# Kernel tuning notes

Hardware: AMD Instinct MI355X
Metric: run time of the kernel (lower is better)

## Reference

```python
import jax, jax.numpy as jnp
import numpy as np

D_IN = 1024
D_OUT = 1024
NUM_HEADS = 16
HEAD_DIM = D_OUT // NUM_HEADS


def setup_inputs() -> dict:
    key = jax.random.key(0)
    ks = jax.random.split(key, 9)
    s = 0.02
    return {
        "x": jax.random.normal(ks[0], (2, 2048, D_IN), dtype=jnp.float32),
        "Wq": jax.random.normal(ks[1], (D_IN, D_OUT), dtype=jnp.float32) * s,
        "bq": jnp.zeros((D_OUT,), dtype=jnp.float32),
        "Wk": jax.random.normal(ks[2], (D_IN, D_OUT), dtype=jnp.float32) * s,
        "bk": jnp.zeros((D_OUT,), dtype=jnp.float32),
        "Wv": jax.random.normal(ks[3], (D_IN, D_OUT), dtype=jnp.float32) * s,
        "bv": jnp.zeros((D_OUT,), dtype=jnp.float32),
        "Wo": jax.random.normal(ks[4], (D_OUT, D_OUT), dtype=jnp.float32) * s,
        "bo": jnp.zeros((D_OUT,), dtype=jnp.float32),
    }


def reference(x, Wq, bq, Wk, bk, Wv, bv, Wo, bo):
    B, S, _ = x.shape
    H, Dh = NUM_HEADS, HEAD_DIM
    q = (x @ Wq + bq).reshape(B, S, H, Dh).transpose(0, 2, 1, 3)  # bhsd
    k = (x @ Wk + bk).reshape(B, S, H, Dh).transpose(0, 2, 1, 3)
    v = (x @ Wv + bv).reshape(B, S, H, Dh).transpose(0, 2, 1, 3)
    scores = jnp.einsum("bhqd,bhkd->bhqk", q, k) * (Dh ** -0.5)
    causal = jnp.tril(jnp.ones((S, S), dtype=bool))
    scores = jnp.where(causal, scores, jnp.float32(-jnp.inf))
    w = jax.nn.softmax(scores, axis=-1)
    ctx = jnp.einsum("bhqk,bhkd->bhqd", w, v)
    ctx = ctx.transpose(0, 2, 1, 3).reshape(B, S, H * Dh)
    return ctx @ Wo + bo
```

## Files before the change

kernel.cpp:

```cpp
#include <hip/hip_runtime.h>
#include <cmath>

#define D_IN 1024
#define D_OUT 1024
#define NUM_HEADS 16
#define HEAD_DIM 64
#define BATCH 2
#define SEQ 2048
#define GK 1024
#define KT 32
#define NT_K (GK / 64)

typedef __attribute__((ext_vector_type(8))) short short8;
typedef __attribute__((ext_vector_type(4))) short short4v;
typedef __attribute__((ext_vector_type(4))) float float4v;
typedef __attribute__((ext_vector_type(16))) float f32x16;
typedef __attribute__((ext_vector_type(2))) int int2v;

__device__ __forceinline__ unsigned short f2bf(float f) {
  unsigned int u = __builtin_bit_cast(unsigned int, f);
  unsigned int r = (u + 0x7FFFu + ((u >> 16) & 1u)) >> 16;
  return (unsigned short)r;
}
__device__ __forceinline__ float bf2f(unsigned short h) {
  return __builtin_bit_cast(float, (unsigned int)h << 16);
}

__device__ __forceinline__ unsigned int cvtpk(float lo, float hi) {
  unsigned int r;
  asm("v_cvt_pk_bf16_f32 %0, %1, %2" : "=v"(r) : "v"(lo), "v"(hi));
  return r;
}

__device__ __forceinline__ void async_copy16(void* lds, const void* g) {
  __builtin_amdgcn_global_load_lds(
      (const __attribute__((address_space(1))) unsigned int*)g,
      (__attribute__((address_space(3))) unsigned int*)lds, 16, 0, 0);
}

__global__ __launch_bounds__(256) void prep(
    const float* __restrict__ x, const float* __restrict__ Wq,
    const float* __restrict__ Wk, const float* __restrict__ Wv,
    const float* __restrict__ Wo, unsigned short* __restrict__ xb,
    unsigned short* __restrict__ wqkv_t, unsigned short* __restrict__ wo_t) {
  const int z = blockIdx.z;
  if (z == 4) {
    const int bid = blockIdx.y * 32 + blockIdx.x;
    const size_t i0 = ((size_t)bid * 256 + threadIdx.x) * 16;
#pragma unroll
    for (int half = 0; half < 2; ++half) {
      const size_t o = i0 + half * 8;
      float4 a = *(const float4*)(x + o);
      float4 b = *(const float4*)(x + o + 4);
      union { unsigned int d[4]; short8 v; } t;
      t.d[0] = cvtpk(a.x, a.y); t.d[1] = cvtpk(a.z, a.w);
      t.d[2] = cvtpk(b.x, b.y); t.d[3] = cvtpk(b.z, b.w);
      *(short8*)(xb + o) = t.v;
    }
    return;
  }
  const float* W = (z == 0) ? Wq : (z == 1) ? Wk : (z == 2) ? Wv : Wo;
  unsigned short* out = (z < 3) ? (wqkv_t + (size_t)z * 1024 * 1024) : wo_t;

  __shared__ float T[32][33];
  const int r = threadIdx.x >> 3;
  const int c4 = (threadIdx.x & 7) << 2;
  const int k0 = blockIdx.x * 32, n0 = blockIdx.y * 32;

  float4 v = *(const float4*)(W + (size_t)(k0 + r) * 1024 + n0 + c4);
  T[r][c4 + 0] = v.x; T[r][c4 + 1] = v.y; T[r][c4 + 2] = v.z; T[r][c4 + 3] = v.w;
  __syncthreads();

  union { unsigned short u[4]; short4v v4; } o;
#pragma unroll
  for (int i = 0; i < 4; ++i) o.u[i] = f2bf(T[c4 + i][r]);
  *(short4v*)(out + (size_t)(n0 + r) * 1024 + k0 + c4) = o.v4;
}

__device__ __forceinline__ void stage_tile(
    const unsigned short* __restrict__ A, const unsigned short* __restrict__ Bt,
    unsigned short* S, int buf, int bm, int bn, int k0, int wave, int lane) {
  unsigned short* As = S + buf * 16384;
  unsigned short* Bs = As + 8192;
#pragma unroll
  for (int t = 0; t < 4; ++t) {
    const int c = (wave * 4 + t) * 64 + lane;
    const int srow = c >> 3;
    const int sgc = ((c & 7) ^ (srow & 7)) * 8;
    async_copy16(As + (size_t)c * 8, A + (size_t)(bm + srow) * GK + k0 + sgc);
  }
#pragma unroll
  for (int t = 0; t < 4; ++t) {
    const int c = (wave * 4 + t) * 64 + lane;
    const int srow = c >> 3;
    const int sgc = ((c & 7) ^ (srow & 7)) * 8;
    async_copy16(Bs + (size_t)c * 8, Bt + (size_t)(bn + srow) * GK + k0 + sgc);
  }
}

__device__ __forceinline__ void gemm_core(
    const unsigned short* __restrict__ A, const unsigned short* __restrict__ Bt,
    unsigned short* S, int bm, int bn, float4v acc[4][4]) {
  const int tid = threadIdx.x;
  const int wave = tid >> 6, lane = tid & 63;
  const int quad = lane >> 4, l16 = lane & 15;
  const int wr = wave >> 1, wc = wave & 1;
  const int sw = l16 & 7;

  stage_tile(A, Bt, S, 0, bm, bn, 0, wave, lane);

  for (int t = 0; t < NT_K; ++t) {
    if (t + 1 < NT_K) {
      stage_tile(A, Bt, S, (t + 1) & 1, bm, bn, (t + 1) * 64, wave, lane);
      asm volatile("s_waitcnt vmcnt(8)" ::: "memory");
    } else {
      asm volatile("s_waitcnt vmcnt(0)" ::: "memory");
    }
    __builtin_amdgcn_sched_barrier(0);
    __builtin_amdgcn_s_barrier();
    __builtin_amdgcn_sched_barrier(0);

    const unsigned short* Asc = S + (t & 1) * 16384;
    const unsigned short* Bsc = Asc + 8192;
#pragma unroll
    for (int h = 0; h < 2; ++h) {
      short8 af[4], bfr[4];
#pragma unroll
      for (int i = 0; i < 4; ++i) {
        const int row = wr * 64 + i * 16 + l16;
        af[i] = *(const short8*)&Asc[((size_t)row * 8 + ((h * 4 + quad) ^ sw)) * 8];
      }
#pragma unroll
      for (int j = 0; j < 4; ++j) {
        const int row = wc * 64 + j * 16 + l16;
        bfr[j] = *(const short8*)&Bsc[((size_t)row * 8 + ((h * 4 + quad) ^ sw)) * 8];
      }
#pragma unroll
      for (int i = 0; i < 4; ++i)
#pragma unroll
        for (int j = 0; j < 4; ++j)
          acc[i][j] = __builtin_amdgcn_mfma_f32_16x16x32_bf16(af[i], bfr[j], acc[i][j], 0, 0, 0);
    }

    __builtin_amdgcn_sched_barrier(0);
    __builtin_amdgcn_s_barrier();
    __builtin_amdgcn_sched_barrier(0);
  }
}

__global__ __launch_bounds__(256) void gemm_qkv(
    const unsigned short* __restrict__ A, const unsigned short* __restrict__ Bt,
    const float* __restrict__ bq, const float* __restrict__ bk,
    const float* __restrict__ bv,
    unsigned short* __restrict__ qbuf, unsigned short* __restrict__ kblk,
    unsigned short* __restrict__ vblk) {
  __shared__ unsigned short SMEM[2 * 128 * 64 * 2];
  const int tid = threadIdx.x;
  const int wave = tid >> 6, lane = tid & 63;
  const int quad = lane >> 4, l16 = lane & 15;
  const int wr = wave >> 1, wc = wave & 1;

  const int lid = blockIdx.y * 32 + blockIdx.x;
  const int nid = (lid & 7) * 96 + (lid >> 3);
  const int bm = (nid & 31) * 128, bn = (nid >> 5) * 128;

  float4v acc[4][4] = {};
  gemm_core(A, Bt, SMEM, bm, bn, acc);

  __syncthreads();

  const int seg = bn >> 10;
  const int nb0 = bn & 1023;
  const float* bias = (seg == 0) ? bq : (seg == 1) ? bk : bv;
  const float scale = (seg == 0) ? 0.18033688011112043f : 1.0f;

#pragma unroll
  for (int j = 0; j < 4; ++j) {
    const int nl = wc * 64 + j * 16 + l16;
    const float bsv = bias[nb0 + nl];
#pragma unroll
    for (int i = 0; i < 4; ++i) {
#pragma unroll
      for (int r = 0; r < 4; ++r) {
        const int ml = wr * 64 + i * 16 + quad * 4 + r;
        SMEM[ml * 136 + nl] = f2bf((acc[i][j][r] + bsv) * scale);
      }
    }
  }
  __syncthreads();

  const int b = bm >> 11;
  const int s0 = bm & 2047;

  if (seg == 0) {
#pragma unroll
    for (int it = 0; it < 8; ++it) {
      const int linear = it * 256 + tid;
      const int d3 = linear & 7;
      const int sl = (linear >> 3) & 127;
      const int h = linear >> 10;
      const short8 vv = *(const short8*)&SMEM[sl * 136 + h * 64 + d3 * 8];
      const int bh = b * NUM_HEADS + (nb0 >> 6) + h;
      *(short8*)&qbuf[((size_t)bh * SEQ + s0 + sl) * HEAD_DIM + d3 * 8] = vv;
    }
  } else if (seg == 1) {
#pragma unroll
    for (int it = 0; it < 8; ++it) {
      const int linear = it * 256 + tid;
      const int key = linear & 31;
      const int hb = (linear >> 5) & 1;
      const int f = (linear >> 6) & 3;
      const int st = (linear >> 8) & 3;
      const int h = linear >> 10;
      const int ml = st * 32 + key;
      const int nl = h * 64 + f * 16 + hb * 8;
      const short8 vv = *(const short8*)&SMEM[ml * 136 + nl];
      const int bh = b * NUM_HEADS + (nb0 >> 6) + h;
      const int stg = (s0 >> 5) + st;
      *(short8*)&kblk[((size_t)bh * 64 + stg) * 2048 + f * 512 + hb * 256 + key * 8] = vv;
    }
  } else {
#pragma unroll
    for (int it = 0; it < 8; ++it) {
      const int linear = it * 256 + tid;
      const int d31 = linear & 31;
      const int s8 = (linear >> 5) & 1;
      const int dt = (linear >> 6) & 1;
      const int kk = (linear >> 7) & 1;
      const int st = (linear >> 8) & 3;
      const int h = linear >> 10;
      const int nl = h * 64 + dt * 32 + d31;
      const int mlb = st * 32 + kk * 16 + s8 * 8;
      union { unsigned short u[8]; short8 v; } vv;
#pragma unroll
      for (int s0i = 0; s0i < 8; ++s0i)
        vv.u[s0i] = SMEM[(mlb + s0i) * 136 + nl];
      const int bh = b * NUM_HEADS + (nb0 >> 6) + h;
      const int stg = (s0 >> 5) + st;
      *(short8*)&vblk[((size_t)bh * 64 + stg) * 2048 + (kk * 2 + dt) * 512 +
                      s8 * 256 + d31 * 8] = vv.v;
    }
  }
}

__global__ __launch_bounds__(256) void gemm_out(
    const unsigned short* __restrict__ A, const unsigned short* __restrict__ Bt,
    const float* __restrict__ bo, float* __restrict__ out) {
  __shared__ unsigned short S[2 * 128 * 64 * 2];
  const int wave = threadIdx.x >> 6, lane = threadIdx.x & 63;
  const int quad = lane >> 4, l16 = lane & 15;
  const int wr = wave >> 1, wc = wave & 1;

  const int lid = blockIdx.y * 32 + blockIdx.x;
  const int nid = (lid & 7) * 32 + (lid >> 3);
  const int bm = (nid & 31) * 128, bn = (nid >> 5) * 128;

  float4v acc[4][4] = {};
  gemm_core(A, Bt, S, bm, bn, acc);

#pragma unroll
  for (int j = 0; j < 4; ++j) {
    const int n = bn + wc * 64 + j * 16 + l16;
    const float bsv = bo[n];
#pragma unroll
    for (int i = 0; i < 4; ++i) {
#pragma unroll
      for (int r = 0; r < 4; ++r) {
        const int m = bm + wr * 64 + i * 16 + quad * 4 + r;
        out[(size_t)m * D_OUT + n] = acc[i][j][r] + bsv;
      }
    }
  }
}

#define OBS 72

__global__ __launch_bounds__(256) void attn_kernel(
    const unsigned short* __restrict__ qf, const unsigned short* __restrict__ kblk,
    const unsigned short* __restrict__ vblk, unsigned short* __restrict__ ctx) {
  __shared__ unsigned short OB[4 * 64 * OBS];
  __shared__ float LL[4 * 64];

  const int id = blockIdx.x;
  const int bh = id & 31;
  const int pr = id >> 5;
  const int a = pr;
  const int b = 63 - pr;
  const int tid = threadIdx.x;
  const int w = tid >> 6;
  const int lane = tid & 63;
  const int l32 = lane & 31;
  const int hi = lane >> 5;

  const size_t bh_base = (size_t)bh * SEQ * HEAD_DIM;
  const unsigned short* kb = kblk + bh_base + (size_t)lane * 8;
  const unsigned short* vb = vblk + bh_base + (size_t)lane * 8;

  short8 qfr[2][4];
  {
    const int q0[2] = {a * 32, b * 32};
#pragma unroll
    for (int qt = 0; qt < 2; ++qt) {
      const unsigned short* qrow =
          qf + bh_base + (size_t)(q0[qt] + l32) * HEAD_DIM + hi * 8;
#pragma unroll
      for (int f = 0; f < 4; ++f) qfr[qt][f] = *(const short8*)(qrow + f * 16);
    }
  }

  f32x16 O[2][2] = {};
  float l_part[2] = {};

  {
    short8 kA[4], vA[4], kB[4], vB[4];

    auto load = [&](int kt, short8 kd[4], short8 vd[4]) {
      const size_t base = (size_t)kt * 2048;
#pragma unroll
      for (int f = 0; f < 4; ++f) kd[f] = *(const short8*)(kb + base + f * 512);
#pragma unroll
      for (int f = 0; f < 4; ++f) vd[f] = *(const short8*)(vb + base + f * 512);
    };

    auto unit = [&](int qt, bool masked, const short8 kd[4], const short8 vd[4]) {
      f32x16 s = {};
#pragma unroll
      for (int f = 0; f < 4; ++f)
        s = __builtin_amdgcn_mfma_f32_32x32x16_bf16(kd[f], qfr[qt][f], s, 0, 0, 0);

      float p[16];
#pragma unroll
      for (int g = 0; g < 4; ++g)
#pragma unroll
        for (int r = 0; r < 4; ++r) {
          float sv = s[g * 4 + r];
          if (masked) {
            const int krow = r + 8 * g + 4 * hi;
            sv = (krow <= l32) ? sv : -1e30f;
          }
          const float pv = __builtin_exp2f(sv);
          p[g * 4 + r] = pv;
          l_part[qt] += pv;
        }

      unsigned int c[8];
#pragma unroll
      for (int g = 0; g < 4; ++g) {
        c[g * 2 + 0] = cvtpk(p[g * 4 + 0], p[g * 4 + 1]);
        c[g * 2 + 1] = cvtpk(p[g * 4 + 2], p[g * 4 + 3]);
      }
      {
        int2v r0 = __builtin_amdgcn_permlane32_swap((int)c[0], (int)c[2], false, false);
        c[0] = (unsigned int)r0.x; c[2] = (unsigned int)r0.y;
        int2v r1 = __builtin_amdgcn_permlane32_swap((int)c[1], (int)c[3], false, false);
        c[1] = (unsigned int)r1.x; c[3] = (unsigned int)r1.y;
        int2v r2 = __builtin_amdgcn_permlane32_swap((int)c[4], (int)c[6], false, false);
        c[4] = (unsigned int)r2.x; c[6] = (unsigned int)r2.y;
        int2v r3 = __builtin_amdgcn_permlane32_swap((int)c[5], (int)c[7], false, false);
        c[5] = (unsigned int)r3.x; c[7] = (unsigned int)r3.y;
      }
      union { unsigned int d[4]; short8 v; } pa0, pa1;
      pa0.d[0] = c[0]; pa0.d[1] = c[1]; pa0.d[2] = c[2]; pa0.d[3] = c[3];
      pa1.d[0] = c[4]; pa1.d[1] = c[5]; pa1.d[2] = c[6]; pa1.d[3] = c[7];

      O[qt][0] = __builtin_amdgcn_mfma_f32_32x32x16_bf16(pa0.v, vd[0], O[qt][0], 0, 0, 0);
      O[qt][1] = __builtin_amdgcn_mfma_f32_32x32x16_bf16(pa0.v, vd[1], O[qt][1], 0, 0, 0);
      O[qt][0] = __builtin_amdgcn_mfma_f32_32x32x16_bf16(pa1.v, vd[2], O[qt][0], 0, 0, 0);
      O[qt][1] = __builtin_amdgcn_mfma_f32_32x32x16_bf16(pa1.v, vd[3], O[qt][1], 0, 0, 0);
    };

    auto step = [&](int kt, const short8 kd[4], const short8 vd[4]) {
      unit(1, kt == b, kd, vd);
      if (kt <= a) unit(0, kt == a, kd, vd);
    };

    load(w, kA, vA);
    int kt = w;
    while (true) {
      const bool lastA = (kt + 4 > b);
      if (!lastA) load(kt + 4, kB, vB);
      step(kt, kA, vA);
      if (lastA) break;
      kt += 4;
      const bool lastB = (kt + 4 > b);
      if (!lastB) load(kt + 4, kA, vA);
      step(kt, kB, vB);
      if (lastB) break;
      kt += 4;
    }
  }

#pragma unroll
  for (int qt = 0; qt < 2; ++qt) {
    const float lsum = l_part[qt] + __shfl_xor(l_part[qt], 32);
    if (hi == 0) LL[w * 64 + qt * 32 + l32] = lsum;
#pragma unroll
    for (int g = 0; g < 4; ++g)
#pragma unroll
      for (int r = 0; r < 4; ++r) {
        const int reg = g * 4 + r;
        const int row = qt * 32 + r + 8 * g + 4 * hi;
        OB[(w * 64 + row) * OBS + l32] = f2bf(O[qt][0][reg]);
        OB[(w * 64 + row) * OBS + 32 + l32] = f2bf(O[qt][1][reg]);
      }
  }

  __syncthreads();

  const int bb = bh >> 4, h = bh & 15;
#pragma unroll
  for (int rep = 0; rep < 2; ++rep) {
    const int idx = rep * 256 + tid;
    const int row = idx >> 3;
    const int col0 = (idx & 7) * 8;
    float acc[8] = {};
#pragma unroll
    for (int u = 0; u < 4; ++u) {
      const short8 t = *(const short8*)&OB[(u * 64 + row) * OBS + col0];
#pragma unroll
      for (int i = 0; i < 8; ++i) acc[i] += bf2f((unsigned short)t[i]);
    }
    const float inv =
        1.0f / (LL[row] + LL[64 + row] + LL[128 + row] + LL[192 + row]);
    union { unsigned short u[8]; short8 v; } o;
#pragma unroll
    for (int i = 0; i < 8; ++i) o.u[i] = f2bf(acc[i] * inv);
    const int qg = (row < 32) ? (a * 32 + row) : (b * 32 + row - 32);
    *(short8*)(ctx + ((size_t)bb * SEQ + qg) * D_OUT + h * HEAD_DIM + col0) = o.v;
  }
}

extern "C" void kernel_launch(void* const* d_in, const int* in_sizes, int n_in,
                              void* d_out, int out_size, void* d_ws, size_t ws_size,
                              hipStream_t stream) {
  const float* x  = (const float*)d_in[0];
  const float* Wq = (const float*)d_in[1];
  const float* bq = (const float*)d_in[2];
  const float* Wk = (const float*)d_in[3];
  const float* bk = (const float*)d_in[4];
  const float* Wv = (const float*)d_in[5];
  const float* bv = (const float*)d_in[6];
  const float* Wo = (const float*)d_in[7];
  const float* bo = (const float*)d_in[8];
  float* out = (float*)d_out;

  const int M = BATCH * SEQ;
  unsigned short* xb     = (unsigned short*)d_ws;
  unsigned short* wqkv_t = xb + (size_t)M * D_IN;
  unsigned short* wo_t   = wqkv_t + (size_t)3 * D_OUT * D_IN;
  unsigned short* qb     = wo_t + (size_t)D_OUT * D_OUT;
  unsigned short* kblk   = qb + (size_t)M * D_OUT;
  unsigned short* vblk   = kblk + (size_t)M * D_OUT;
  unsigned short* cb     = vblk + (size_t)M * D_OUT;

  prep<<<dim3(32, 32, 5), 256, 0, stream>>>(x, Wq, Wk, Wv, Wo, xb, wqkv_t, wo_t);
  gemm_qkv<<<dim3(M / 128, 3 * D_OUT / 128), 256, 0, stream>>>(
      xb, wqkv_t, bq, bk, bv, qb, kblk, vblk);
  attn_kernel<<<dim3(32 * 32), 256, 0, stream>>>(qb, kblk, vblk, cb);
  gemm_out<<<dim3(M / 128, D_OUT / 128), 256, 0, stream>>>(cb, wo_t, bo, out);
}
```

Baseline: 182.5 us.

## Shrink GEMM K-tile to 32 and compute softmax row sums with MFMA

The shared GEMM core now stages 32-wide K tiles, with no XOR swizzle, across 32 steps instead of 64-wide tiles across 16. This halves LDS use, which could allow more blocks per CU, but doubles the barrier count and may add LDS bank conflicts on the unswizzled 64-byte rows. Separately, the attention kernel no longer sums exp values with per-lane scalar adds. It accumulates row sums with extra MFMAs against a bf16 ones vector, which moves VALU work onto the matrix unit but sums the bf16-rounded probabilities rather than the fp32 ones.

```diff
diff --git a/kernel.cpp b/kernel.cpp
--- a/kernel.cpp
+++ b/kernel.cpp
@@ -9,7 +9,8 @@
 #define SEQ 2048
 #define GK 1024
 #define KT 32
-#define NT_K (GK / 64)
+#define BK 32
+#define NSTEP (GK / BK)
 
 typedef __attribute__((ext_vector_type(8))) short short8;
 typedef __attribute__((ext_vector_type(4))) short short4v;
@@ -79,22 +80,20 @@
 
 __device__ __forceinline__ void stage_tile(
     const unsigned short* __restrict__ A, const unsigned short* __restrict__ Bt,
-    unsigned short* S, int buf, int bm, int bn, int k0, int wave, int lane) {
-  unsigned short* As = S + buf * 16384;
-  unsigned short* Bs = As + 8192;
-#pragma unroll
-  for (int t = 0; t < 4; ++t) {
-    const int c = (wave * 4 + t) * 64 + lane;
-    const int srow = c >> 3;
-    const int sgc = ((c & 7) ^ (srow & 7)) * 8;
-    async_copy16(As + (size_t)c * 8, A + (size_t)(bm + srow) * GK + k0 + sgc);
-  }
-#pragma unroll
-  for (int t = 0; t < 4; ++t) {
-    const int c = (wave * 4 + t) * 64 + lane;
-    const int srow = c >> 3;
-    const int sgc = ((c & 7) ^ (srow & 7)) * 8;
-    async_copy16(Bs + (size_t)c * 8, Bt + (size_t)(bn + srow) * GK + k0 + sgc);
+    unsigned short* S, int buf, int bm, int bn, int k0, int tid) {
+  unsigned short* As = S + buf * 8192;
+  unsigned short* Bs = As + 4096;
+#pragma unroll
+  for (int t = 0; t < 2; ++t) {
+    const int c = t * 256 + tid;
+    const int row = c >> 2, oct = c & 3;
+    async_copy16(As + (size_t)c * 8, A + (size_t)(bm + row) * GK + k0 + oct * 8);
+  }
+#pragma unroll
+  for (int t = 0; t < 2; ++t) {
+    const int c = t * 256 + tid;
+    const int row = c >> 2, oct = c & 3;
+    async_copy16(Bs + (size_t)c * 8, Bt + (size_t)(bn + row) * GK + k0 + oct * 8);
   }
 }
 
@@ -105,14 +104,13 @@
   const int wave = tid >> 6, lane = tid & 63;
   const int quad = lane >> 4, l16 = lane & 15;
   const int wr = wave >> 1, wc = wave & 1;
-  const int sw = l16 & 7;
-
-  stage_tile(A, Bt, S, 0, bm, bn, 0, wave, lane);
-
-  for (int t = 0; t < NT_K; ++t) {
-    if (t + 1 < NT_K) {
-      stage_tile(A, Bt, S, (t + 1) & 1, bm, bn, (t + 1) * 64, wave, lane);
-      asm volatile("s_waitcnt vmcnt(8)" ::: "memory");
+
+  stage_tile(A, Bt, S, 0, bm, bn, 0, tid);
+
+  for (int t = 0; t < NSTEP; ++t) {
+    if (t + 1 < NSTEP) {
+      stage_tile(A, Bt, S, (t + 1) & 1, bm, bn, (t + 1) * BK, tid);
+      asm volatile("s_waitcnt vmcnt(4)" ::: "memory");
     } else {
       asm volatile("s_waitcnt vmcnt(0)" ::: "memory");
     }
@@ -120,27 +118,24 @@
     __builtin_amdgcn_s_barrier();
     __builtin_amdgcn_sched_barrier(0);
 
-    const unsigned short* Asc = S + (t & 1) * 16384;
-    const unsigned short* Bsc = Asc + 8192;
-#pragma unroll
-    for (int h = 0; h < 2; ++h) {
-      short8 af[4], bfr[4];
-#pragma unroll
-      for (int i = 0; i < 4; ++i) {
-        const int row = wr * 64 + i * 16 + l16;
-        af[i] = *(const short8*)&Asc[((size_t)row * 8 + ((h * 4 + quad) ^ sw)) * 8];
-      }
-#pragma unroll
-      for (int j = 0; j < 4; ++j) {
-        const int row = wc * 64 + j * 16 + l16;
-        bfr[j] = *(const short8*)&Bsc[((size_t)row * 8 + ((h * 4 + quad) ^ sw)) * 8];
-      }
-#pragma unroll
-      for (int i = 0; i < 4; ++i)
-#pragma unroll
-        for (int j = 0; j < 4; ++j)
-          acc[i][j] = __builtin_amdgcn_mfma_f32_16x16x32_bf16(af[i], bfr[j], acc[i][j], 0, 0, 0);
-    }
+    const unsigned short* Asc = S + (t & 1) * 8192;
+    const unsigned short* Bsc = Asc + 4096;
+    short8 af[4], bfr[4];
+#pragma unroll
+    for (int i = 0; i < 4; ++i) {
+      const int row = wr * 64 + i * 16 + l16;
+      af[i] = *(const short8*)&Asc[(size_t)(row * 4 + quad) * 8];
+    }
+#pragma unroll
+    for (int j = 0; j < 4; ++j) {
+      const int row = wc * 64 + j * 16 + l16;
+      bfr[j] = *(const short8*)&Bsc[(size_t)(row * 4 + quad) * 8];
+    }
+#pragma unroll
+    for (int i = 0; i < 4; ++i)
+#pragma unroll
+      for (int j = 0; j < 4; ++j)
+        acc[i][j] = __builtin_amdgcn_mfma_f32_16x16x32_bf16(af[i], bfr[j], acc[i][j], 0, 0, 0);
 
     __builtin_amdgcn_sched_barrier(0);
     __builtin_amdgcn_s_barrier();
@@ -154,7 +149,7 @@
     const float* __restrict__ bv,
     unsigned short* __restrict__ qbuf, unsigned short* __restrict__ kblk,
     unsigned short* __restrict__ vblk) {
-  __shared__ unsigned short SMEM[2 * 128 * 64 * 2];
+  __shared__ unsigned short SMEM[17408];
   const int tid = threadIdx.x;
   const int wave = tid >> 6, lane = tid & 63;
   const int quad = lane >> 4, l16 = lane & 15;
@@ -246,7 +241,7 @@
 __global__ __launch_bounds__(256) void gemm_out(
     const unsigned short* __restrict__ A, const unsigned short* __restrict__ Bt,
     const float* __restrict__ bo, float* __restrict__ out) {
-  __shared__ unsigned short S[2 * 128 * 64 * 2];
+  __shared__ unsigned short S[16384];
   const int wave = threadIdx.x >> 6, lane = threadIdx.x & 63;
   const int quad = lane >> 4, l16 = lane & 15;
   const int wr = wave >> 1, wc = wave & 1;
@@ -296,6 +291,11 @@
   const unsigned short* kb = kblk + bh_base + (size_t)lane * 8;
   const unsigned short* vb = vblk + bh_base + (size_t)lane * 8;
 
+  union { unsigned short u[8]; short8 v; } onesu;
+#pragma unroll
+  for (int i = 0; i < 8; ++i) onesu.u[i] = 0x3F80;
+  const short8 onesB = onesu.v;
+
   short8 qfr[2][4];
   {
     const int q0[2] = {a * 32, b * 32};
@@ -309,7 +309,7 @@
   }
 
   f32x16 O[2][2] = {};
-  float l_part[2] = {};
+  f32x16 lacc[2] = {};
 
   {
     short8 kA[4], vA[4], kB[4], vB[4];
@@ -338,9 +338,7 @@
             const int krow = r + 8 * g + 4 * hi;
             sv = (krow <= l32) ? sv : -1e30f;
           }
-          const float pv = __builtin_exp2f(sv);
-          p[g * 4 + r] = pv;
-          l_part[qt] += pv;
+          p[g * 4 + r] = __builtin_exp2f(sv);
         }
 
       unsigned int c[8];
@@ -365,8 +363,10 @@
 
       O[qt][0] = __builtin_amdgcn_mfma_f32_32x32x16_bf16(pa0.v, vd[0], O[qt][0], 0, 0, 0);
       O[qt][1] = __builtin_amdgcn_mfma_f32_32x32x16_bf16(pa0.v, vd[1], O[qt][1], 0, 0, 0);
+      lacc[qt] = __builtin_amdgcn_mfma_f32_32x32x16_bf16(pa0.v, onesB, lacc[qt], 0, 0, 0);
       O[qt][0] = __builtin_amdgcn_mfma_f32_32x32x16_bf16(pa1.v, vd[2], O[qt][0], 0, 0, 0);
       O[qt][1] = __builtin_amdgcn_mfma_f32_32x32x16_bf16(pa1.v, vd[3], O[qt][1], 0, 0, 0);
+      lacc[qt] = __builtin_amdgcn_mfma_f32_32x32x16_bf16(pa1.v, onesB, lacc[qt], 0, 0, 0);
     };
 
     auto step = [&](int kt, const short8 kd[4], const short8 vd[4]) {
@@ -390,10 +390,17 @@
     }
   }
 
+  if (l32 == 0) {
+#pragma unroll
+    for (int qt = 0; qt < 2; ++qt)
+#pragma unroll
+      for (int g = 0; g < 4; ++g)
+#pragma unroll
+        for (int r = 0; r < 4; ++r)
+          LL[w * 64 + qt * 32 + r + 8 * g + 4 * hi] = lacc[qt][g * 4 + r];
+  }
 #pragma unroll
   for (int qt = 0; qt < 2; ++qt) {
-    const float lsum = l_part[qt] + __shfl_xor(l_part[qt], 32);
-    if (hi == 0) LL[w * 64 + qt * 32 + l32] = lsum;
 #pragma unroll
     for (int g = 0; g < 4; ++g)
 #pragma unroll
```

Result: slower. 198.3 us (+8.6%).
